# Kernel tuning notes

Hardware: AMD Instinct MI355X
Metric: run time of the kernel (lower is better)

## Reference

```python
import jax, jax.numpy as jnp
import numpy as np

B, T, C, HS = 8, 2048, 2048, 128  # batch, seq, n_embedding, head_size
THETA = 10000.0


def _rope_tables(dim, seq_len, theta=THETA):
    freqs = 1.0 / theta ** (jnp.arange(0, dim, 2, dtype=jnp.float32) / dim)  # [dim/2]
    t = jnp.arange(seq_len, dtype=jnp.float32)
    ang = jnp.outer(t, freqs)  # [T, dim/2]
    return jnp.cos(ang), jnp.sin(ang)


def _apply_rope(v, cos, sin):
    # v: [B,T,D]; pairs along last dim treated as complex (real=even, imag=odd)
    b, t, d = v.shape
    vr = v.reshape(b, t, d // 2, 2)
    x0, x1 = vr[..., 0], vr[..., 1]
    o0 = x0 * cos - x1 * sin
    o1 = x0 * sin + x1 * cos
    return jnp.stack([o0, o1], axis=-1).reshape(b, t, d)


def setup_inputs() -> dict:
    key = jax.random.key(0)
    k1, k2, k3, k4 = jax.random.split(key, 4)
    scale = 1.0 / np.sqrt(C)
    x = jax.random.normal(k1, (B, T, C), dtype=jnp.float32)
    Wk = jax.random.normal(k2, (C, HS), dtype=jnp.float32) * scale
    Wq = jax.random.normal(k3, (C, HS), dtype=jnp.float32) * scale
    Wv = jax.random.normal(k4, (C, HS), dtype=jnp.float32) * scale
    return {"x": x, "Wk": Wk, "Wq": Wq, "Wv": Wv}


def reference(x, Wk, Wq, Wv):
    b, t, _ = x.shape
    cos, sin = _rope_tables(HS, t)
    k = x @ Wk  # [B,T,HS]
    q = x @ Wq
    # Source: xq,xk = apply_rotary_emb(key, query); query,key = xq,xk
    # => scores = rope(q_proj) @ rope(k_proj)^T (standard causal attention)
    qr = _apply_rope(q, cos, sin)
    kr = _apply_rope(k, cos, sin)
    scores = jnp.einsum('btd,bsd->bts', qr, kr) * (HS ** -0.5)  # [B,T,T]
    causal = jnp.tril(jnp.ones((t, t), dtype=bool))
    scores = jnp.where(causal, scores, -jnp.inf)
    wei = jax.nn.softmax(scores, axis=-1)
    v = x @ Wv
    return jnp.einsum('bts,bsd->btd', wei, v)
```

## Files before the change

### kernel.cpp

```cpp
#include <hip/hip_runtime.h>

#define NB 8
#define NT 2048
#define NC 2048
#define NH 128

typedef short s8v __attribute__((ext_vector_type(8)));
typedef float f4  __attribute__((ext_vector_type(4)));

static __device__ __forceinline__ unsigned short f2bf(float f) {
    union { float f; unsigned int u; } v; v.f = f;
    unsigned int x = v.u;
    return (unsigned short)((x + 0x7FFFu + ((x >> 16) & 1u)) >> 16);
}

__global__ __launch_bounds__(256) void wtrans_k(
    const float* __restrict__ Wk, const float* __restrict__ Wq,
    const float* __restrict__ Wv, unsigned short* __restrict__ wt)
{
    __shared__ float Ls[64][129];
    const int mat = blockIdx.y;
    const float* W = (mat == 0) ? Wq : (mat == 1) ? Wk : Wv;
    const int k0 = blockIdx.x * 64;
    const int t  = threadIdx.x;

    #pragma unroll
    for (int j = 0; j < 8; ++j) {
        int flat = j * 1024 + t * 4;
        int k = flat >> 7, n = flat & 127;
        f4 v = *reinterpret_cast<const f4*>(W + (size_t)(k0 + k) * NH + n);
        Ls[k][n] = v[0]; Ls[k][n + 1] = v[1]; Ls[k][n + 2] = v[2]; Ls[k][n + 3] = v[3];
    }
    __syncthreads();

    const int n = t >> 1, half = t & 1;
    unsigned short tmp[32];
    #pragma unroll
    for (int kk = 0; kk < 32; ++kk) tmp[kk] = f2bf(Ls[half * 32 + kk][n]);

    const int nb  = mat * 8 + (n >> 4);
    const int l16 = n & 15;
    const int kbi = blockIdx.x * 2 + half;
    unsigned short* dst = wt + ((size_t)nb * 64 + kbi) * 512;
    #pragma unroll
    for (int v = 0; v < 4; ++v)
        *reinterpret_cast<s8v*>(dst + (v * 16 + l16) * 8) = *reinterpret_cast<s8v*>(tmp + v * 8);
}

__global__ __launch_bounds__(512) void proj_rope(
    const float* __restrict__ x, const unsigned short* __restrict__ wt,
    unsigned short* __restrict__ qws, unsigned short* __restrict__ kws,
    unsigned short* __restrict__ vtws)
{
    __shared__ char ALDS[2][9216];

    const int tid  = threadIdx.x;
    const int wave = tid >> 6;
    const int lane = tid & 63;
    const int quad = lane >> 4, l16 = lane & 15;
    const int wm = wave >> 2, wn = wave & 3;
    const int M0 = blockIdx.x * 64;

    const int srow = tid >> 3, sc = tid & 7;
    const float* xsrc = x + (size_t)(M0 + srow) * NC + sc * 8;
    char* sdst[2] = { &ALDS[0][srow * 144 + sc * 16], &ALDS[1][srow * 144 + sc * 16] };

    const unsigned short* bb[6];
    #pragma unroll
    for (int ni = 0; ni < 6; ++ni)
        bb[ni] = wt + ((size_t)(wn * 6 + ni) * 64) * 512 + lane * 8;

    f4 acc[2][6];
    #pragma unroll
    for (int mi = 0; mi < 2; ++mi)
        #pragma unroll
        for (int ni = 0; ni < 6; ++ni)
            acc[mi][ni] = (f4){0.f, 0.f, 0.f, 0.f};

    f4 rlo = *reinterpret_cast<const f4*>(xsrc);
    f4 rhi = *reinterpret_cast<const f4*>(xsrc + 4);
    {
        union { f4 f; unsigned int u[4]; } L, H; L.f = rlo; H.f = rhi;
        union { s8v s; unsigned int u[4]; } A;
        A.u[0] = __builtin_amdgcn_perm(L.u[1], L.u[0], 0x07060302u);
        A.u[1] = __builtin_amdgcn_perm(L.u[3], L.u[2], 0x07060302u);
        A.u[2] = __builtin_amdgcn_perm(H.u[1], H.u[0], 0x07060302u);
        A.u[3] = __builtin_amdgcn_perm(H.u[3], H.u[2], 0x07060302u);
        *reinterpret_cast<s8v*>(sdst[0]) = A.s;
    }
    rlo = *reinterpret_cast<const f4*>(xsrc + 64);
    rhi = *reinterpret_cast<const f4*>(xsrc + 68);
    __syncthreads();

    for (int t = 0; t < 32; ++t) {
        const char* cur = ALDS[t & 1];
        if (t < 31) {
            union { f4 f; unsigned int u[4]; } L, H; L.f = rlo; H.f = rhi;
            union { s8v s; unsigned int u[4]; } A;
            A.u[0] = __builtin_amdgcn_perm(L.u[1], L.u[0], 0x07060302u);
            A.u[1] = __builtin_amdgcn_perm(L.u[3], L.u[2], 0x07060302u);
            A.u[2] = __builtin_amdgcn_perm(H.u[1], H.u[0], 0x07060302u);
            A.u[3] = __builtin_amdgcn_perm(H.u[3], H.u[2], 0x07060302u);
            *reinterpret_cast<s8v*>(sdst[(t + 1) & 1]) = A.s;
        }
        if (t < 30) {
            rlo = *reinterpret_cast<const f4*>(xsrc + (t + 2) * 64);
            rhi = *reinterpret_cast<const f4*>(xsrc + (t + 2) * 64 + 4);
        }
        #pragma unroll
        for (int ksub = 0; ksub < 2; ++ksub) {
            const int co = (ksub * 4 + quad) * 16;
            s8v a0 = *reinterpret_cast<const s8v*>(cur + (wm * 32 + l16) * 144 + co);
            s8v a1 = *reinterpret_cast<const s8v*>(cur + (wm * 32 + 16 + l16) * 144 + co);
            const size_t kb = (size_t)(t * 2 + ksub) * 512;
            #pragma unroll
            for (int ni = 0; ni < 6; ++ni) {
                s8v b = *reinterpret_cast<const s8v*>(bb[ni] + kb);
                acc[0][ni] = __builtin_amdgcn_mfma_f32_16x16x32_bf16(a0, b, acc[0][ni], 0, 0, 0);
                acc[1][ni] = __builtin_amdgcn_mfma_f32_16x16x32_bf16(a1, b, acc[1][ni], 0, 0, 0);
            }
        }
        __syncthreads();
    }

    const float cfreq = -0.10381025296f;
    #pragma unroll
    for (int mi = 0; mi < 2; ++mi) {
        #pragma unroll
        for (int ni = 0; ni < 6; ++ni) {
            const int outcol = wn * 96 + ni * 16 + l16;
            const int mat = outcol >> 7;
            const int col = outcol & 127;
            #pragma unroll
            for (int r = 0; r < 4; ++r) {
                const int row = M0 + wm * 32 + mi * 16 + quad * 4 + r;
                const int t   = row & (NT - 1);
                float v = acc[mi][ni][r];
                if (mat < 2) {
                    float other = __shfl_xor(v, 1, 64);
                    float freq  = exp2f(cfreq * (float)(col & ~1));
                    float ang   = (float)t * freq;
                    float sn = sinf(ang), cs = cosf(ang);
                    v = (col & 1) ? (other * sn + v * cs)
                                  : (v * cs - other * sn);
                }
                unsigned short bv = f2bf(v);
                if (mat == 0)      qws[(size_t)row * NH + col] = bv;
                else if (mat == 1) kws[(size_t)row * NH + col] = bv;
                else {
                    int b = row >> 11;
                    vtws[(size_t)b * (NH * NT) + (size_t)col * NT + t] = bv;
                }
            }
        }
    }
}

__global__ __launch_bounds__(256, 2) void attn_k(
    const unsigned short* __restrict__ qws, const unsigned short* __restrict__ kws,
    const unsigned short* __restrict__ vtws, float* __restrict__ out)
{
    __shared__ unsigned short P[4][32 * 64];
    __shared__ float Os[4][32][64];
    __shared__ float Ms[4][32], Ls[4][32], Lt[32];

    const int wave = threadIdx.x >> 6;
    const int lane = threadIdx.x & 63;
    const int quad = lane >> 4, l16 = lane & 15;
    const int b     = blockIdx.y;
    const int qrow0 = blockIdx.x * 32;
    const unsigned short* Q  = qws  + (size_t)b * NT * NH;
    const unsigned short* K  = kws  + (size_t)b * NT * NH;
    const unsigned short* Vt = vtws + (size_t)b * NH * NT;

    s8v qf[2][4];
    #pragma unroll
    for (int mi = 0; mi < 2; ++mi)
        #pragma unroll
        for (int ks = 0; ks < 4; ++ks)
            qf[mi][ks] = *reinterpret_cast<const s8v*>(
                Q + (size_t)(qrow0 + mi * 16 + l16) * NH + ks * 32 + quad * 8);

    float m[2][4], ls[2][4];
    f4 o[2][8];
    #pragma unroll
    for (int mi = 0; mi < 2; ++mi) {
        #pragma unroll
        for (int r = 0; r < 4; ++r) { m[mi][r] = -INFINITY; ls[mi][r] = 0.f; }
        #pragma unroll
        for (int dt = 0; dt < 8; ++dt) o[mi][dt] = (f4){0.f, 0.f, 0.f, 0.f};
    }

    const int nkt = (qrow0 >> 6) + 1;
    const float scale2 = 0.1275166948f;

    for (int kt = wave; kt < nkt; kt += 4) {
        const int kbase = kt * 64;
        const bool domask = (kt == nkt - 1);

        f4 s[2][4];
        #pragma unroll
        for (int nt = 0; nt < 4; ++nt) {
            f4 a0 = (f4){0.f, 0.f, 0.f, 0.f}, a1 = a0;
            #pragma unroll
            for (int ks = 0; ks < 4; ++ks) {
                s8v kf = *reinterpret_cast<const s8v*>(
                    K + (size_t)(kbase + nt * 16 + l16) * NH + ks * 32 + quad * 8);
                a0 = __builtin_amdgcn_mfma_f32_16x16x32_bf16(qf[0][ks], kf, a0, 0, 0, 0);
                a1 = __builtin_amdgcn_mfma_f32_16x16x32_bf16(qf[1][ks], kf, a1, 0, 0, 0);
            }
            s[0][nt] = a0; s[1][nt] = a1;
        }

        float tmx[2][4];
        #pragma unroll
        for (int mi = 0; mi < 2; ++mi) {
            #pragma unroll
            for (int r = 0; r < 4; ++r) {
                const int trow = qrow0 + mi * 16 + quad * 4 + r;
                #pragma unroll
                for (int nt = 0; nt < 4; ++nt) {
                    float sv = s[mi][nt][r] * scale2;
                    if (domask && (kbase + nt * 16 + l16 > trow)) sv = -INFINITY;
                    s[mi][nt][r] = sv;
                }
                float tm = fmaxf(fmaxf(s[mi][0][r], s[mi][1][r]),
                                 fmaxf(s[mi][2][r], s[mi][3][r]));
                #pragma unroll
                for (int off = 1; off < 16; off <<= 1)
                    tm = fmaxf(tm, __shfl_xor(tm, off, 64));
                tmx[mi][r] = tm;
            }
        }

        bool grow = false;
        #pragma unroll
        for (int mi = 0; mi < 2; ++mi)
            #pragma unroll
            for (int r = 0; r < 4; ++r)
                grow = grow || (tmx[mi][r] > m[mi][r] + 8.0f);
        if (__any(grow)) {
            #pragma unroll
            for (int mi = 0; mi < 2; ++mi)
                #pragma unroll
                for (int r = 0; r < 4; ++r) {
                    const float mn = fmaxf(m[mi][r], tmx[mi][r]);
                    const float alpha = exp2f(m[mi][r] - mn);
                    m[mi][r] = mn;
                    ls[mi][r] *= alpha;
                    #pragma unroll
                    for (int dt = 0; dt < 8; ++dt) o[mi][dt][r] *= alpha;
                }
        }

        #pragma unroll
        for (int mi = 0; mi < 2; ++mi)
            #pragma unroll
            for (int r = 0; r < 4; ++r) {
                float rs = 0.f;
                #pragma unroll
                for (int nt = 0; nt < 4; ++nt) {
                    float p = exp2f(s[mi][nt][r] - m[mi][r]);
                    s[mi][nt][r] = p;
                    rs += p;
                }
                ls[mi][r] += rs;
            }

        #pragma unroll
        for (int mi = 0; mi < 2; ++mi)
            #pragma unroll
            for (int nt = 0; nt < 4; ++nt)
                #pragma unroll
                for (int r = 0; r < 4; ++r) {
                    const int prow = mi * 16 + quad * 4 + r;
                    const int swz  = ((nt * 2 + (l16 >> 3)) ^ (prow & 7)) * 8 + (l16 & 7);
                    P[wave][prow * 64 + swz] = f2bf(s[mi][nt][r]);
                }

        #pragma unroll
        for (int ks2 = 0; ks2 < 2; ++ks2) {
            s8v pa[2];
            #pragma unroll
            for (int mi = 0; mi < 2; ++mi) {
                const int prow = mi * 16 + l16;
                const int pp = ((ks2 * 4 + quad) ^ (l16 & 7));
                pa[mi] = *reinterpret_cast<const s8v*>(&P[wave][prow * 64 + pp * 8]);
            }
            #pragma unroll
            for (int dt = 0; dt < 8; ++dt) {
                s8v vf = *reinterpret_cast<const s8v*>(
                    Vt + (size_t)(dt * 16 + l16) * NT + kbase + ks2 * 32 + quad * 8);
                o[0][dt] = __builtin_amdgcn_mfma_f32_16x16x32_bf16(pa[0], vf, o[0][dt], 0, 0, 0);
                o[1][dt] = __builtin_amdgcn_mfma_f32_16x16x32_bf16(pa[1], vf, o[1][dt], 0, 0, 0);
            }
        }
    }

    #pragma unroll
    for (int mi = 0; mi < 2; ++mi)
        #pragma unroll
        for (int r = 0; r < 4; ++r) {
            float v = ls[mi][r];
            #pragma unroll
            for (int off = 1; off < 16; off <<= 1) v += __shfl_xor(v, off, 64);
            ls[mi][r] = v;
        }

    if (l16 == 0) {
        #pragma unroll
        for (int mi = 0; mi < 2; ++mi)
            #pragma unroll
            for (int r = 0; r < 4; ++r) {
                Ms[wave][mi * 16 + quad * 4 + r] = m[mi][r];
                Ls[wave][mi * 16 + quad * 4 + r] = ls[mi][r];
            }
    }
    __syncthreads();

    #pragma unroll
    for (int mi = 0; mi < 2; ++mi)
        #pragma unroll
        for (int r = 0; r < 4; ++r) {
            const int row = mi * 16 + quad * 4 + r;
            float M = fmaxf(fmaxf(Ms[0][row], Ms[1][row]), fmaxf(Ms[2][row], Ms[3][row]));
            float sc = exp2f(m[mi][r] - M);
            float lt = Ls[0][row] * exp2f(Ms[0][row] - M) + Ls[1][row] * exp2f(Ms[1][row] - M)
                     + Ls[2][row] * exp2f(Ms[2][row] - M) + Ls[3][row] * exp2f(Ms[3][row] - M);
            if (wave == 0 && l16 == 0) Lt[row] = lt;
            #pragma unroll
            for (int dt = 0; dt < 8; ++dt) o[mi][dt][r] *= sc;
        }

    const int rrow = threadIdx.x >> 3;
    const int cx   = (threadIdx.x & 7) * 8;
    #pragma unroll
    for (int h = 0; h < 2; ++h) {
        __syncthreads();
        #pragma unroll
        for (int mi = 0; mi < 2; ++mi)
            #pragma unroll
            for (int dtl = 0; dtl < 4; ++dtl)
                #pragma unroll
                for (int r = 0; r < 4; ++r)
                    Os[wave][mi * 16 + quad * 4 + r][dtl * 16 + l16] = o[mi][h * 4 + dtl][r];
        __syncthreads();
        f4 s0 = (f4){0.f, 0.f, 0.f, 0.f}, s1 = s0;
        #pragma unroll
        for (int w = 0; w < 4; ++w) {
            s0 += *reinterpret_cast<const f4*>(&Os[w][rrow][cx]);
            s1 += *reinterpret_cast<const f4*>(&Os[w][rrow][cx + 4]);
        }
        const float rl = 1.0f / Lt[rrow];
        float* dst = &out[((size_t)b * NT + qrow0 + rrow) * NH + h * 64 + cx];
        *reinterpret_cast<f4*>(dst)     = s0 * rl;
        *reinterpret_cast<f4*>(dst + 4) = s1 * rl;
    }
}

extern "C" void kernel_launch(void* const* d_in, const int* in_sizes, int n_in,
                              void* d_out, int out_size, void* d_ws, size_t ws_size,
                              hipStream_t stream) {
    const float* x  = (const float*)d_in[0];
    const float* Wk = (const float*)d_in[1];
    const float* Wq = (const float*)d_in[2];
    const float* Wv = (const float*)d_in[3];
    unsigned short* ws   = (unsigned short*)d_ws;
    unsigned short* wt   = ws;
    unsigned short* qws  = ws  + 786432;
    unsigned short* kws  = qws + 2097152;
    unsigned short* vtws = kws + 2097152;
    float* outp = (float*)d_out;

    wtrans_k<<<dim3(32, 3), 256, 0, stream>>>(Wk, Wq, Wv, wt);
    proj_rope<<<dim3(256), 512, 0, stream>>>(x, wt, qws, kws, vtws);
    attn_k<<<dim3(64, 8), 256, 0, stream>>>(qws, kws, vtws, outp);
}
```

Measured before the change: 335.9 us.

## Store Q/K/V in MFMA-fragment-packed layout and register-prefetch weights in projection

The projection kernel now writes Q, K and V directly in a tile-packed layout that matches the MFMA operand fragments. This lets the attention kernel load each fragment as one contiguous 16-byte-per-lane read instead of strided row or column reads. The projection main loop is also unrolled by two, with the weight fragments prefetched into registers one step ahead so global loads overlap the MFMAs. In exchange the projection epilogue does more scattered small stores and uses more registers for the double-buffered weights.

```diff
diff --git a/kernel.cpp b/kernel.cpp
--- a/kernel.cpp
+++ b/kernel.cpp
@@ -6,12 +6,23 @@
 #define NH 128
 
 typedef short s8v __attribute__((ext_vector_type(8)));
+typedef short s4v __attribute__((ext_vector_type(4)));
 typedef float f4  __attribute__((ext_vector_type(4)));
 
 static __device__ __forceinline__ unsigned short f2bf(float f) {
     union { float f; unsigned int u; } v; v.f = f;
     unsigned int x = v.u;
     return (unsigned short)((x + 0x7FFFu + ((x >> 16) & 1u)) >> 16);
+}
+
+static __device__ __forceinline__ s8v pack8(f4 lo, f4 hi) {
+    union { f4 f; unsigned int u[4]; } L, H; L.f = lo; H.f = hi;
+    union { s8v s; unsigned int u[4]; } A;
+    A.u[0] = __builtin_amdgcn_perm(L.u[1], L.u[0], 0x07060302u);
+    A.u[1] = __builtin_amdgcn_perm(L.u[3], L.u[2], 0x07060302u);
+    A.u[2] = __builtin_amdgcn_perm(H.u[1], H.u[0], 0x07060302u);
+    A.u[3] = __builtin_amdgcn_perm(H.u[3], H.u[2], 0x07060302u);
+    return A.s;
 }
 
 __global__ __launch_bounds__(256) void wtrans_k(
@@ -49,8 +60,8 @@
 
 __global__ __launch_bounds__(512) void proj_rope(
     const float* __restrict__ x, const unsigned short* __restrict__ wt,
-    unsigned short* __restrict__ qws, unsigned short* __restrict__ kws,
-    unsigned short* __restrict__ vtws)
+    unsigned short* __restrict__ qp, unsigned short* __restrict__ kp,
+    unsigned short* __restrict__ vp)
 {
     __shared__ char ALDS[2][9216];
 
@@ -63,12 +74,10 @@
 
     const int srow = tid >> 3, sc = tid & 7;
     const float* xsrc = x + (size_t)(M0 + srow) * NC + sc * 8;
-    char* sdst[2] = { &ALDS[0][srow * 144 + sc * 16], &ALDS[1][srow * 144 + sc * 16] };
-
-    const unsigned short* bb[6];
-    #pragma unroll
-    for (int ni = 0; ni < 6; ++ni)
-        bb[ni] = wt + ((size_t)(wn * 6 + ni) * 64) * 512 + lane * 8;
+    char* sd0 = &ALDS[0][srow * 144 + sc * 16];
+    char* sd1 = &ALDS[1][srow * 144 + sc * 16];
+
+    const unsigned short* wtb = wt + (size_t)(wn * 6) * 32768 + lane * 8;
 
     f4 acc[2][6];
     #pragma unroll
@@ -77,53 +86,83 @@
         for (int ni = 0; ni < 6; ++ni)
             acc[mi][ni] = (f4){0.f, 0.f, 0.f, 0.f};
 
-    f4 rlo = *reinterpret_cast<const f4*>(xsrc);
-    f4 rhi = *reinterpret_cast<const f4*>(xsrc + 4);
-    {
-        union { f4 f; unsigned int u[4]; } L, H; L.f = rlo; H.f = rhi;
-        union { s8v s; unsigned int u[4]; } A;
-        A.u[0] = __builtin_amdgcn_perm(L.u[1], L.u[0], 0x07060302u);
-        A.u[1] = __builtin_amdgcn_perm(L.u[3], L.u[2], 0x07060302u);
-        A.u[2] = __builtin_amdgcn_perm(H.u[1], H.u[0], 0x07060302u);
-        A.u[3] = __builtin_amdgcn_perm(H.u[3], H.u[2], 0x07060302u);
-        *reinterpret_cast<s8v*>(sdst[0]) = A.s;
-    }
-    rlo = *reinterpret_cast<const f4*>(xsrc + 64);
-    rhi = *reinterpret_cast<const f4*>(xsrc + 68);
+    s8v bcur[2][6], bnxt[2][6];
+
+    f4 a0lo = *reinterpret_cast<const f4*>(xsrc);
+    f4 a0hi = *reinterpret_cast<const f4*>(xsrc + 4);
+    f4 a1lo = *reinterpret_cast<const f4*>(xsrc + 64);
+    f4 a1hi = *reinterpret_cast<const f4*>(xsrc + 68);
+    #pragma unroll
+    for (int ks = 0; ks < 2; ++ks)
+        #pragma unroll
+        for (int ni = 0; ni < 6; ++ni)
+            bcur[ks][ni] = *reinterpret_cast<const s8v*>(wtb + (size_t)ni * 32768 + (size_t)ks * 512);
+    *reinterpret_cast<s8v*>(sd0) = pack8(a0lo, a0hi);
+    a0lo = *reinterpret_cast<const f4*>(xsrc + 128);
+    a0hi = *reinterpret_cast<const f4*>(xsrc + 132);
     __syncthreads();
 
-    for (int t = 0; t < 32; ++t) {
-        const char* cur = ALDS[t & 1];
-        if (t < 31) {
-            union { f4 f; unsigned int u[4]; } L, H; L.f = rlo; H.f = rhi;
-            union { s8v s; unsigned int u[4]; } A;
-            A.u[0] = __builtin_amdgcn_perm(L.u[1], L.u[0], 0x07060302u);
-            A.u[1] = __builtin_amdgcn_perm(L.u[3], L.u[2], 0x07060302u);
-            A.u[2] = __builtin_amdgcn_perm(H.u[1], H.u[0], 0x07060302u);
-            A.u[3] = __builtin_amdgcn_perm(H.u[3], H.u[2], 0x07060302u);
-            *reinterpret_cast<s8v*>(sdst[(t + 1) & 1]) = A.s;
-        }
-        if (t < 30) {
-            rlo = *reinterpret_cast<const f4*>(xsrc + (t + 2) * 64);
-            rhi = *reinterpret_cast<const f4*>(xsrc + (t + 2) * 64 + 4);
-        }
+    for (int tt = 0; tt < 16; ++tt) {
+        *reinterpret_cast<s8v*>(sd1) = pack8(a1lo, a1hi);
+        if (tt < 15) {
+            a1lo = *reinterpret_cast<const f4*>(xsrc + (size_t)(2 * tt + 3) * 64);
+            a1hi = *reinterpret_cast<const f4*>(xsrc + (size_t)(2 * tt + 3) * 64 + 4);
+        }
+        #pragma unroll
+        for (int ks = 0; ks < 2; ++ks)
+            #pragma unroll
+            for (int ni = 0; ni < 6; ++ni)
+                bnxt[ks][ni] = *reinterpret_cast<const s8v*>(
+                    wtb + (size_t)ni * 32768 + (size_t)((2 * tt + 1) * 2 + ks) * 512);
         #pragma unroll
         for (int ksub = 0; ksub < 2; ++ksub) {
-            const int co = (ksub * 4 + quad) * 16;
-            s8v a0 = *reinterpret_cast<const s8v*>(cur + (wm * 32 + l16) * 144 + co);
-            s8v a1 = *reinterpret_cast<const s8v*>(cur + (wm * 32 + 16 + l16) * 144 + co);
-            const size_t kb = (size_t)(t * 2 + ksub) * 512;
+            const char* cur = ALDS[0];
+            s8v a0 = *reinterpret_cast<const s8v*>(cur + (wm * 32 + l16) * 144 + (ksub * 4 + quad) * 16);
+            s8v a1 = *reinterpret_cast<const s8v*>(cur + (wm * 32 + 16 + l16) * 144 + (ksub * 4 + quad) * 16);
             #pragma unroll
             for (int ni = 0; ni < 6; ++ni) {
-                s8v b = *reinterpret_cast<const s8v*>(bb[ni] + kb);
-                acc[0][ni] = __builtin_amdgcn_mfma_f32_16x16x32_bf16(a0, b, acc[0][ni], 0, 0, 0);
-                acc[1][ni] = __builtin_amdgcn_mfma_f32_16x16x32_bf16(a1, b, acc[1][ni], 0, 0, 0);
+                acc[0][ni] = __builtin_amdgcn_mfma_f32_16x16x32_bf16(a0, bcur[ksub][ni], acc[0][ni], 0, 0, 0);
+                acc[1][ni] = __builtin_amdgcn_mfma_f32_16x16x32_bf16(a1, bcur[ksub][ni], acc[1][ni], 0, 0, 0);
             }
         }
         __syncthreads();
+
+        if (tt < 15) {
+            *reinterpret_cast<s8v*>(sd0) = pack8(a0lo, a0hi);
+            if (tt < 14) {
+                a0lo = *reinterpret_cast<const f4*>(xsrc + (size_t)(2 * tt + 4) * 64);
+                a0hi = *reinterpret_cast<const f4*>(xsrc + (size_t)(2 * tt + 4) * 64 + 4);
+            }
+            #pragma unroll
+            for (int ks = 0; ks < 2; ++ks)
+                #pragma unroll
+                for (int ni = 0; ni < 6; ++ni)
+                    bcur[ks][ni] = *reinterpret_cast<const s8v*>(
+                        wtb + (size_t)ni * 32768 + (size_t)((2 * tt + 2) * 2 + ks) * 512);
+        }
+        #pragma unroll
+        for (int ksub = 0; ksub < 2; ++ksub) {
+            const char* cur = ALDS[1];
+            s8v a0 = *reinterpret_cast<const s8v*>(cur + (wm * 32 + l16) * 144 + (ksub * 4 + quad) * 16);
+            s8v a1 = *reinterpret_cast<const s8v*>(cur + (wm * 32 + 16 + l16) * 144 + (ksub * 4 + quad) * 16);
+            #pragma unroll
+            for (int ni = 0; ni < 6; ++ni) {
+                acc[0][ni] = __builtin_amdgcn_mfma_f32_16x16x32_bf16(a0, bnxt[ksub][ni], acc[0][ni], 0, 0, 0);
+                acc[1][ni] = __builtin_amdgcn_mfma_f32_16x16x32_bf16(a1, bnxt[ksub][ni], acc[1][ni], 0, 0, 0);
+            }
+        }
+        __syncthreads();
     }
 
     const float cfreq = -0.10381025296f;
+    const int tb  = M0 >> 11;
+    const int tl  = M0 & 2047;
+    unsigned short* qpB = qp + (size_t)tb * 262144;
+    unsigned short* kpB = kp + (size_t)tb * 262144;
+    unsigned short* vpB = vp + (size_t)tb * 262144;
+    const int qt0 = (tl >> 5) + wm;
+    const int kt0 = tl >> 6;
+
     #pragma unroll
     for (int mi = 0; mi < 2; ++mi) {
         #pragma unroll
@@ -131,10 +170,10 @@
             const int outcol = wn * 96 + ni * 16 + l16;
             const int mat = outcol >> 7;
             const int col = outcol & 127;
+            float vv[4];
             #pragma unroll
             for (int r = 0; r < 4; ++r) {
-                const int row = M0 + wm * 32 + mi * 16 + quad * 4 + r;
-                const int t   = row & (NT - 1);
+                const int t = tl + wm * 32 + mi * 16 + quad * 4 + r;
                 float v = acc[mi][ni][r];
                 if (mat < 2) {
                     float other = __shfl_xor(v, 1, 64);
@@ -144,21 +183,37 @@
                     v = (col & 1) ? (other * sn + v * cs)
                                   : (v * cs - other * sn);
                 }
-                unsigned short bv = f2bf(v);
-                if (mat == 0)      qws[(size_t)row * NH + col] = bv;
-                else if (mat == 1) kws[(size_t)row * NH + col] = bv;
-                else {
-                    int b = row >> 11;
-                    vtws[(size_t)b * (NH * NT) + (size_t)col * NT + t] = bv;
-                }
+                vv[r] = v;
+            }
+            if (mat == 0) {
+                const int ks = col >> 5, qq = (col >> 3) & 3, e = col & 7;
+                unsigned short* d = qpB + ((((size_t)qt0 * 2 + mi) * 4 + ks) * 64 + qq * 16 + quad * 4) * 8 + e;
+                #pragma unroll
+                for (int r = 0; r < 4; ++r) d[r * 8] = f2bf(vv[r]);
+            } else if (mat == 1) {
+                const int ks = col >> 5, qq = (col >> 3) & 3, e = col & 7;
+                const int nt = wm * 2 + mi;
+                unsigned short* d = kpB + ((((size_t)kt0 * 4 + nt) * 4 + ks) * 64 + qq * 16 + quad * 4) * 8 + e;
+                #pragma unroll
+                for (int r = 0; r < 4; ++r) d[r * 8] = f2bf(vv[r]);
+            } else {
+                const int dt  = col >> 4;
+                const int ks2 = wm;
+                const int qv  = mi * 2 + (quad >> 1);
+                const int e4  = (quad & 1) * 4;
+                unsigned short* d = vpB + ((((size_t)kt0 * 2 + ks2) * 8 + dt) * 64 + qv * 16 + l16) * 8 + e4;
+                s4v pk;
+                #pragma unroll
+                for (int r = 0; r < 4; ++r) pk[r] = (short)f2bf(vv[r]);
+                *reinterpret_cast<s4v*>(d) = pk;
             }
         }
     }
 }
 
 __global__ __launch_bounds__(256, 2) void attn_k(
-    const unsigned short* __restrict__ qws, const unsigned short* __restrict__ kws,
-    const unsigned short* __restrict__ vtws, float* __restrict__ out)
+    const unsigned short* __restrict__ qp, const unsigned short* __restrict__ kp,
+    const unsigned short* __restrict__ vp, float* __restrict__ out)
 {
     __shared__ unsigned short P[4][32 * 64];
     __shared__ float Os[4][32][64];
@@ -169,9 +224,10 @@
     const int quad = lane >> 4, l16 = lane & 15;
     const int b     = blockIdx.y;
     const int qrow0 = blockIdx.x * 32;
-    const unsigned short* Q  = qws  + (size_t)b * NT * NH;
-    const unsigned short* K  = kws  + (size_t)b * NT * NH;
-    const unsigned short* Vt = vtws + (size_t)b * NH * NT;
+    const int qt    = blockIdx.x;
+    const unsigned short* Qp = qp + (size_t)b * 262144;
+    const unsigned short* Kp = kp + (size_t)b * 262144;
+    const unsigned short* Vp = vp + (size_t)b * 262144;
 
     s8v qf[2][4];
     #pragma unroll
@@ -179,7 +235,7 @@
         #pragma unroll
         for (int ks = 0; ks < 4; ++ks)
             qf[mi][ks] = *reinterpret_cast<const s8v*>(
-                Q + (size_t)(qrow0 + mi * 16 + l16) * NH + ks * 32 + quad * 8);
+                Qp + ((((size_t)qt * 2 + mi) * 4 + ks) * 64 + lane) * 8);
 
     float m[2][4], ls[2][4];
     f4 o[2][8];
@@ -197,6 +253,8 @@
     for (int kt = wave; kt < nkt; kt += 4) {
         const int kbase = kt * 64;
         const bool domask = (kt == nkt - 1);
+        const unsigned short* Kt = Kp + (size_t)kt * 8192;
+        const unsigned short* Vt = Vp + (size_t)kt * 8192;
 
         f4 s[2][4];
         #pragma unroll
@@ -204,8 +262,7 @@
             f4 a0 = (f4){0.f, 0.f, 0.f, 0.f}, a1 = a0;
             #pragma unroll
             for (int ks = 0; ks < 4; ++ks) {
-                s8v kf = *reinterpret_cast<const s8v*>(
-                    K + (size_t)(kbase + nt * 16 + l16) * NH + ks * 32 + quad * 8);
+                s8v kf = *reinterpret_cast<const s8v*>(Kt + (((nt * 4 + ks) * 64) + lane) * 8);
                 a0 = __builtin_amdgcn_mfma_f32_16x16x32_bf16(qf[0][ks], kf, a0, 0, 0, 0);
                 a1 = __builtin_amdgcn_mfma_f32_16x16x32_bf16(qf[1][ks], kf, a1, 0, 0, 0);
             }
@@ -289,8 +346,7 @@
             }
             #pragma unroll
             for (int dt = 0; dt < 8; ++dt) {
-                s8v vf = *reinterpret_cast<const s8v*>(
-                    Vt + (size_t)(dt * 16 + l16) * NT + kbase + ks2 * 32 + quad * 8);
+                s8v vf = *reinterpret_cast<const s8v*>(Vt + (((ks2 * 8 + dt) * 64) + lane) * 8);
                 o[0][dt] = __builtin_amdgcn_mfma_f32_16x16x32_bf16(pa[0], vf, o[0][dt], 0, 0, 0);
                 o[1][dt] = __builtin_amdgcn_mfma_f32_16x16x32_bf16(pa[1], vf, o[1][dt], 0, 0, 0);
             }
```

Result: faster. 285.3 us (-15.1%).
